# Kernel tuning notes

Hardware: AMD Instinct MI355X
Metric: run time of the kernel (lower is better)

The kernel has to match this reference:

```python
import jax, jax.numpy as jnp
import numpy as np

KH = KW = 3
PAD = 1
STRIDE = 1
C_IN = 32
C_OUT = 16
H = W = 64
B = 64
H_OUT = (H - KH + 2 * PAD) // STRIDE + 1
W_OUT = (W - KW + 2 * PAD) // STRIDE + 1
S = H_OUT * W_OUT
K = C_IN * KH * KW


def unfold_2d(x):
    # x: [B, C, H, W] -> [B, C*KH*KW, S], torch.nn.functional.unfold ordering
    xp = jnp.pad(x, ((0, 0), (0, 0), (PAD, PAD), (PAD, PAD)))
    patches = []
    for i in range(KH):
        for j in range(KW):
            patches.append(xp[:, :, i:i + H_OUT * STRIDE:STRIDE, j:j + W_OUT * STRIDE:STRIDE])
    u = jnp.stack(patches, axis=2)  # [B, C, KH*KW, H_OUT, W_OUT]
    return u.reshape(x.shape[0], K, S)


def setup_inputs() -> dict:
    key = jax.random.key(0)
    k1, k2, k3 = jax.random.split(key, 3)
    X = jax.random.normal(k1, (B, C_IN, H, W), dtype=jnp.float32)
    # kaiming normal (linear): std = 1/sqrt(fan_in), fan_in = K for each location's GEMM
    weight = jax.random.normal(k2, (S, K, C_OUT), dtype=jnp.float32) / jnp.sqrt(jnp.float32(K))
    # xavier uniform over [H_OUT, W_OUT]
    lim = np.sqrt(6.0 / (H_OUT + W_OUT))
    bias = jax.random.uniform(k3, (H_OUT, W_OUT), dtype=jnp.float32, minval=-lim, maxval=lim)
    return {"X": X, "weight": weight, "bias": bias}


def reference(X, weight, bias):
    ufld = unfold_2d(X)                               # [B, K, S]
    ufld = ufld + bias.reshape(1, 1, -1)              # bias added per-location to patches
    h = jnp.einsum('bks,skc->bcs', ufld, weight)      # per-location unshared GEMM
    return h.reshape(X.shape[0], C_OUT, H_OUT, W_OUT)
```

## Files before the change

kernel.cpp:

```cpp
#include <hip/hip_runtime.h>
#include <stdint.h>
#include <stddef.h>

#define HOUT 64
#define WOUT 64
#define CIN  32
#define COUT 16
#define SLOC 4096
#define KTOT 288
#define HPAD 66
#define WPAD 148

typedef __attribute__((ext_vector_type(8))) short  short8;
typedef __attribute__((ext_vector_type(4))) float  floatx4;
typedef __attribute__((ext_vector_type(2))) float  floatx2;

static __device__ __forceinline__ unsigned short f2bf(float f) {
    union { float f; unsigned int u; } v; v.f = f;
    unsigned int u = v.u;
    unsigned int r = (u + 0x7FFFu + ((u >> 16) & 1u)) >> 16;
    return (unsigned short)r;
}

static __device__ __forceinline__ unsigned int cvt_pk_bf16(float lo, float hi) {
    unsigned int r;
    asm("v_cvt_pk_bf16_f32 %0, %1, %2" : "=v"(r) : "v"(lo), "v"(hi));
    return r;
}

__global__ __launch_bounds__(256) void prep_kernel(const float* __restrict__ X,
                                                   unsigned short* __restrict__ xt) {
    const int id  = blockIdx.x;
    const int tid = threadIdx.x;

    if (id < 260) {
        int h1, w1;
        if (id < 66)       { h1 = 0;  w1 = id; }
        else if (id < 132) { h1 = 65; w1 = id - 66; }
        else { int r = id - 132; h1 = (r >> 1) + 1; w1 = (r & 1) ? 65 : 0; }
        ((uint4*)(xt + (size_t)(h1 * HPAD + w1) * 2048))[tid] = uint4{0u, 0u, 0u, 0u};
    }

    const int w   = tid >> 2;
    const int cg8 = (tid & 3) * 8;
#pragma unroll
    for (int u = 0; u < 2; ++u) {
        const int unit = id * 2 + u;
        const int h = unit >> 6, b = unit & 63;
        const float* xb = X + (((size_t)b * CIN + cg8) * HOUT + h) * WOUT + w;
        unsigned short v[8];
#pragma unroll
        for (int j = 0; j < 8; ++j)
            v[j] = f2bf(xb[(size_t)j * HOUT * WOUT]);
        uint4 pack;
        pack.x = (unsigned)v[0] | ((unsigned)v[1] << 16);
        pack.y = (unsigned)v[2] | ((unsigned)v[3] << 16);
        pack.z = (unsigned)v[4] | ((unsigned)v[5] << 16);
        pack.w = (unsigned)v[6] | ((unsigned)v[7] << 16);
        *(uint4*)(xt + (size_t)((h + 1) * HPAD + (w + 1)) * 2048 + b * CIN + cg8) = pack;
    }
}

__global__ __launch_bounds__(256, 4) void varconv_kernel(const unsigned short* __restrict__ xt,
                                                         const float* __restrict__ Wg,
                                                         const float* __restrict__ bias,
                                                         float* __restrict__ out) {
    __shared__ __align__(16) unsigned int wru[2][16 * WPAD];

    const int id   = blockIdx.x;
    const int sg   = (id & 7) * 256 + (id >> 3);
    const int s0   = sg * 2;
    const int y    = s0 >> 6;
    const int x0   = s0 & 63;
    const int tid  = threadIdx.x;
    const int lane = tid & 63;
    const int wv   = tid >> 6;
    const int q    = lane >> 4;
    const int n    = lane & 15;
    const int B0   = wv * 16;

    const float bias0 = bias[s0];
    const float bias1 = bias[s0 + 1];

    const uint4* wsrc = (const uint4*)(Wg + (size_t)s0 * (KTOT * COUT));
    uint4 fA[5], fB[5];
#pragma unroll
    for (int it = 0; it < 5; ++it) {
        const int tau  = tid + it * 256;
        const int tt   = tau < 1152 ? tau : 1151;
        const int site = tt >= 576;
        const int t2   = tt - 576 * site;
        const int ng = t2 & 3, cp = (t2 >> 2) & 15, t = t2 >> 6;
        const int kA = 18 * cp + t;
        fA[it] = wsrc[site * 1152 + kA * 4 + ng];
        fB[it] = wsrc[site * 1152 + (kA + 9) * 4 + ng];
    }

    const unsigned short* abase = xt + (size_t)(B0 + n) * CIN + q * 8;
    short8 af[3][4];
#pragma unroll
    for (int cy = 0; cy < 3; ++cy)
#pragma unroll
        for (int cx = 0; cx < 4; ++cx)
            af[cy][cx] = *(const short8*)(abase + (size_t)((y + cy) * HPAD + (x0 + cx)) * 2048);

#pragma unroll
    for (int it = 0; it < 5; ++it) {
        const int tau = tid + it * 256;
        if (tau < 1152) {
            const int site = tau >= 576;
            const int t2   = tau - 576 * site;
            const int ng = t2 & 3, cp = (t2 >> 2) & 15, t = t2 >> 6;
            union { uint4 u; float f[4]; } a, b;
            a.u = fA[it]; b.u = fB[it];
            unsigned int* wb = &wru[site][t * 16 + cp];
#pragma unroll
            for (int m = 0; m < 4; ++m)
                wb[(4 * ng + m) * WPAD] = cvt_pk_bf16(a.f[m], b.f[m]);
        }
    }

    __syncthreads();

    const short one = (short)0x3F80;
    const short8 ones = {one, one, one, one, one, one, one, one};
    floatx4 acc0  = {0.f, 0.f, 0.f, 0.f};
    floatx4 acc1  = {0.f, 0.f, 0.f, 0.f};
    floatx4 accc0 = {0.f, 0.f, 0.f, 0.f};
    floatx4 accc1 = {0.f, 0.f, 0.f, 0.f};
    const unsigned int* w0 = &wru[0][n * WPAD + 4 * q];
    const unsigned int* w1 = &wru[1][n * WPAD + 4 * q];
#pragma unroll
    for (int t = 0; t < 9; ++t) {
        const int cy = t / 3, cx = t % 3;
        const short8 b0 = *(const short8*)(w0 + t * 16);
        acc0  = __builtin_amdgcn_mfma_f32_16x16x32_bf16(af[cy][cx], b0, acc0, 0, 0, 0);
        accc0 = __builtin_amdgcn_mfma_f32_16x16x32_bf16(ones, b0, accc0, 0, 0, 0);
        const short8 b1 = *(const short8*)(w1 + t * 16);
        acc1  = __builtin_amdgcn_mfma_f32_16x16x32_bf16(af[cy][cx + 1], b1, acc1, 0, 0, 0);
        accc1 = __builtin_amdgcn_mfma_f32_16x16x32_bf16(ones, b1, accc1, 0, 0, 0);
    }

#pragma unroll
    for (int r = 0; r < 4; ++r) {
        const int b = B0 + 4 * q + r;
        float* dst = out + ((size_t)(b * COUT + n)) * SLOC + s0;
        *(floatx2*)dst = floatx2{acc0[r] + bias0 * accc0[r],
                                 acc1[r] + bias1 * accc1[r]};
    }
}

extern "C" void kernel_launch(void* const* d_in, const int* in_sizes, int n_in,
                              void* d_out, int out_size, void* d_ws, size_t ws_size,
                              hipStream_t stream) {
    const float* X    = (const float*)d_in[0];
    const float* Wg   = (const float*)d_in[1];
    const float* bias = (const float*)d_in[2];
    float* out = (float*)d_out;

    unsigned short* xt = (unsigned short*)d_ws;

    prep_kernel<<<2048, 256, 0, stream>>>(X, xt);
    varconv_kernel<<<2048, 256, 0, stream>>>(xt, Wg, bias, out);
}
```

Baseline: 159.0 us.

## Process four spatial sites per block with wider stores and remapped prep order

Each varconv block now handles four adjacent output locations instead of two, halving the grid and reusing the loaded activation window (3x6 instead of 3x4 fragments). Weights for the four sites are staged in LDS over two sequential load/convert rounds, the inline-asm bf16 pack is replaced by a software round-to-nearest conversion, and outputs are written as 16-byte float4 stores. The prep kernel's block-to-row mapping is also permuted. The aim is to amortise activation loads and raise store width, at the cost of doubled LDS per block and more registers, which may reduce occupancy.

```diff
diff --git a/kernel.cpp b/kernel.cpp
--- a/kernel.cpp
+++ b/kernel.cpp
@@ -13,19 +13,12 @@
 
 typedef __attribute__((ext_vector_type(8))) short  short8;
 typedef __attribute__((ext_vector_type(4))) float  floatx4;
-typedef __attribute__((ext_vector_type(2))) float  floatx2;
 
 static __device__ __forceinline__ unsigned short f2bf(float f) {
     union { float f; unsigned int u; } v; v.f = f;
     unsigned int u = v.u;
     unsigned int r = (u + 0x7FFFu + ((u >> 16) & 1u)) >> 16;
     return (unsigned short)r;
-}
-
-static __device__ __forceinline__ unsigned int cvt_pk_bf16(float lo, float hi) {
-    unsigned int r;
-    asm("v_cvt_pk_bf16_f32 %0, %1, %2" : "=v"(r) : "v"(lo), "v"(hi));
-    return r;
 }
 
 __global__ __launch_bounds__(256) void prep_kernel(const float* __restrict__ X,
@@ -43,15 +36,17 @@
 
     const int w   = tid >> 2;
     const int cg8 = (tid & 3) * 8;
+    const int k   = id & 7;
+    const int j   = id >> 3;
 #pragma unroll
     for (int u = 0; u < 2; ++u) {
-        const int unit = id * 2 + u;
+        const int unit = k * 512 + j * 2 + u;
         const int h = unit >> 6, b = unit & 63;
         const float* xb = X + (((size_t)b * CIN + cg8) * HOUT + h) * WOUT + w;
         unsigned short v[8];
 #pragma unroll
-        for (int j = 0; j < 8; ++j)
-            v[j] = f2bf(xb[(size_t)j * HOUT * WOUT]);
+        for (int jj = 0; jj < 8; ++jj)
+            v[jj] = f2bf(xb[(size_t)jj * HOUT * WOUT]);
         uint4 pack;
         pack.x = (unsigned)v[0] | ((unsigned)v[1] << 16);
         pack.y = (unsigned)v[2] | ((unsigned)v[3] << 16);
@@ -65,11 +60,11 @@
                                                          const float* __restrict__ Wg,
                                                          const float* __restrict__ bias,
                                                          float* __restrict__ out) {
-    __shared__ __align__(16) unsigned int wru[2][16 * WPAD];
+    __shared__ __align__(16) unsigned int wru[4][16 * WPAD];
 
     const int id   = blockIdx.x;
-    const int sg   = (id & 7) * 256 + (id >> 3);
-    const int s0   = sg * 2;
+    const int sg   = (id & 7) * 128 + (id >> 3);
+    const int s0   = sg * 4;
     const int y    = s0 >> 6;
     const int x0   = s0 & 63;
     const int tid  = threadIdx.x;
@@ -79,74 +74,98 @@
     const int n    = lane & 15;
     const int B0   = wv * 16;
 
-    const float bias0 = bias[s0];
-    const float bias1 = bias[s0 + 1];
+    const uint4* wsrc = (const uint4*)(Wg + (size_t)s0 * (KTOT * COUT));
 
-    const uint4* wsrc = (const uint4*)(Wg + (size_t)s0 * (KTOT * COUT));
     uint4 fA[5], fB[5];
-#pragma unroll
-    for (int it = 0; it < 5; ++it) {
-        const int tau  = tid + it * 256;
-        const int tt   = tau < 1152 ? tau : 1151;
-        const int site = tt >= 576;
-        const int t2   = tt - 576 * site;
-        const int ng = t2 & 3, cp = (t2 >> 2) & 15, t = t2 >> 6;
-        const int kA = 18 * cp + t;
-        fA[it] = wsrc[site * 1152 + kA * 4 + ng];
-        fB[it] = wsrc[site * 1152 + (kA + 9) * 4 + ng];
+#define WISSUE(ROUND)                                                          \
+    _Pragma("unroll")                                                          \
+    for (int it = 0; it < 5; ++it) {                                           \
+        const int tau  = tid + it * 256;               \
+        const int tt   = tau < 1152 ? tau : 1151;           \
+        const int site = (tt >= 576) + 2 * (ROUND);                            \
+        const int t2   = tt - 576 * (tt >= 576);                               \
+        const int ng = t2 & 3, cp = (t2 >> 2) & 15, t = t2 >> 6;               \
+        const int kA = 18 * cp + t;                \
+        fA[it] = wsrc[site * 1152 + kA * 4 + ng];                              \
+        fB[it] = wsrc[site * 1152 + (kA + 9) * 4 + ng];                        \
     }
 
+#define WSCATTER(ROUND)                                                        \
+    _Pragma("unroll")                                                          \
+    for (int it = 0; it < 5; ++it) {                                           \
+        const int tau = tid + it * 256;                                        \
+        if (tau < 1152) {                                                      \
+            const int site = (tau >= 576) + 2 * (ROUND);                       \
+            const int t2   = tau - 576 * (tau >= 576);                         \
+            const int ng = t2 & 3, cp = (t2 >> 2) & 15, t = t2 >> 6;           \
+            union { uint4 u; float f[4]; } a, b;                               \
+            a.u = fA[it]; b.u = fB[it];                                        \
+            unsigned int* wb = &wru[site][t * 16 + cp];                        \
+            _Pragma("unroll")                                                  \
+            for (int m = 0; m < 4; ++m)                                        \
+                wb[(4 * ng + m) * WPAD] =                                      \
+                    (unsigned)f2bf(a.f[m]) | ((unsigned)f2bf(b.f[m]) << 16);   \
+        }                                                                      \
+    }
+
+    WISSUE(0)
+
     const unsigned short* abase = xt + (size_t)(B0 + n) * CIN + q * 8;
-    short8 af[3][4];
+    short8 af[3][6];
 #pragma unroll
     for (int cy = 0; cy < 3; ++cy)
 #pragma unroll
-        for (int cx = 0; cx < 4; ++cx)
+        for (int cx = 0; cx < 6; ++cx)
             af[cy][cx] = *(const short8*)(abase + (size_t)((y + cy) * HPAD + (x0 + cx)) * 2048);
 
-#pragma unroll
-    for (int it = 0; it < 5; ++it) {
-        const int tau = tid + it * 256;
-        if (tau < 1152) {
-            const int site = tau >= 576;
-            const int t2   = tau - 576 * site;
-            const int ng = t2 & 3, cp = (t2 >> 2) & 15, t = t2 >> 6;
-            union { uint4 u; float f[4]; } a, b;
-            a.u = fA[it]; b.u = fB[it];
-            unsigned int* wb = &wru[site][t * 16 + cp];
-#pragma unroll
-            for (int m = 0; m < 4; ++m)
-                wb[(4 * ng + m) * WPAD] = cvt_pk_bf16(a.f[m], b.f[m]);
-        }
-    }
+    WSCATTER(0)
+
+    WISSUE(1)
+    WSCATTER(1)
+#undef WISSUE
+#undef WSCATTER
 
     __syncthreads();
 
     const short one = (short)0x3F80;
     const short8 ones = {one, one, one, one, one, one, one, one};
-    floatx4 acc0  = {0.f, 0.f, 0.f, 0.f};
-    floatx4 acc1  = {0.f, 0.f, 0.f, 0.f};
-    floatx4 accc0 = {0.f, 0.f, 0.f, 0.f};
-    floatx4 accc1 = {0.f, 0.f, 0.f, 0.f};
+    floatx4 acc0  = {0.f, 0.f, 0.f, 0.f}, accc0 = {0.f, 0.f, 0.f, 0.f};
+    floatx4 acc1  = {0.f, 0.f, 0.f, 0.f}, accc1 = {0.f, 0.f, 0.f, 0.f};
+    floatx4 acc2  = {0.f, 0.f, 0.f, 0.f}, accc2 = {0.f, 0.f, 0.f, 0.f};
+    floatx4 acc3  = {0.f, 0.f, 0.f, 0.f}, accc3 = {0.f, 0.f, 0.f, 0.f};
     const unsigned int* w0 = &wru[0][n * WPAD + 4 * q];
     const unsigned int* w1 = &wru[1][n * WPAD + 4 * q];
+    const unsigned int* w2 = &wru[2][n * WPAD + 4 * q];
+    const unsigned int* w3 = &wru[3][n * WPAD + 4 * q];
 #pragma unroll
     for (int t = 0; t < 9; ++t) {
         const int cy = t / 3, cx = t % 3;
         const short8 b0 = *(const short8*)(w0 + t * 16);
-        acc0  = __builtin_amdgcn_mfma_f32_16x16x32_bf16(af[cy][cx], b0, acc0, 0, 0, 0);
-        accc0 = __builtin_amdgcn_mfma_f32_16x16x32_bf16(ones, b0, accc0, 0, 0, 0);
+        acc0  = __builtin_amdgcn_mfma_f32_16x16x32_bf16(af[cy][cx],     b0, acc0,  0, 0, 0);
+        accc0 = __builtin_amdgcn_mfma_f32_16x16x32_bf16(ones,           b0, accc0, 0, 0, 0);
         const short8 b1 = *(const short8*)(w1 + t * 16);
-        acc1  = __builtin_amdgcn_mfma_f32_16x16x32_bf16(af[cy][cx + 1], b1, acc1, 0, 0, 0);
-        accc1 = __builtin_amdgcn_mfma_f32_16x16x32_bf16(ones, b1, accc1, 0, 0, 0);
+        acc1  = __builtin_amdgcn_mfma_f32_16x16x32_bf16(af[cy][cx + 1], b1, acc1,  0, 0, 0);
+        accc1 = __builtin_amdgcn_mfma_f32_16x16x32_bf16(ones,           b1, accc1, 0, 0, 0);
+        const short8 b2 = *(const short8*)(w2 + t * 16);
+        acc2  = __builtin_amdgcn_mfma_f32_16x16x32_bf16(af[cy][cx + 2], b2, acc2,  0, 0, 0);
+        accc2 = __builtin_amdgcn_mfma_f32_16x16x32_bf16(ones,           b2, accc2, 0, 0, 0);
+        const short8 b3 = *(const short8*)(w3 + t * 16);
+        acc3  = __builtin_amdgcn_mfma_f32_16x16x32_bf16(af[cy][cx + 3], b3, acc3,  0, 0, 0);
+        accc3 = __builtin_amdgcn_mfma_f32_16x16x32_bf16(ones,           b3, accc3, 0, 0, 0);
     }
+    const float bias0 = bias[s0];
+    const float bias1 = bias[s0 + 1];
+    const float bias2 = bias[s0 + 2];
+    const float bias3 = bias[s0 + 3];
 
 #pragma unroll
     for (int r = 0; r < 4; ++r) {
         const int b = B0 + 4 * q + r;
         float* dst = out + ((size_t)(b * COUT + n)) * SLOC + s0;
-        *(floatx2*)dst = floatx2{acc0[r] + bias0 * accc0[r],
-                                 acc1[r] + bias1 * accc1[r]};
+        *(floatx4*)dst = floatx4{acc0[r] + bias0 * accc0[r],
+                                 acc1[r] + bias1 * accc1[r],
+                                 acc2[r] + bias2 * accc2[r],
+                                 acc3[r] + bias3 * accc3[r]};
     }
 }
 
@@ -161,5 +180,5 @@
     unsigned short* xt = (unsigned short*)d_ws;
 
     prep_kernel<<<2048, 256, 0, stream>>>(X, xt);
-    varconv_kernel<<<2048, 256, 0, stream>>>(xt, Wg, bias, out);
+    varconv_kernel<<<1024, 256, 0, stream>>>(xt, Wg, bias, out);
 }
```

New measurement: 156.9 us. Within noise of the previous version (-1.3%).
